# Kernel optimization log

Measured on AMD Instinct MI355X. Metric: run time of the kernel, lower is better.

Reference implementation:

```python
import jax, jax.numpy as jnp
import numpy as np

B, S, HID, NH, K = 4, 1500, 1024, 16, 64
DH = HID // NH  # 64


def _rel_bias(pos_emb, length):
    # pos_emb: [2K+1, d]; Shaw-style relative position embedding lookup -> [S, S, d]
    kk = (pos_emb.shape[0] - 1) // 2
    idx = jnp.arange(length)
    dist = jnp.clip(idx[None, :] - idx[:, None], -kk, kk) + kk
    return pos_emb[dist]


def setup_inputs() -> dict:
    key = jax.random.key(0)
    ks = jax.random.split(key, 12)
    sq = 1.0 / np.sqrt(HID)
    inp = {
        "query": jax.random.normal(ks[0], (B, S, HID), jnp.float32),
        "key": jax.random.normal(ks[1], (B, S, HID), jnp.float32),
        "value": jax.random.normal(ks[2], (B, S, HID), jnp.float32),
        # per-head QKV projections stacked over heads: [NH, HID, DH]
        "Wq": jax.random.normal(ks[3], (NH, HID, DH), jnp.float32) * sq,
        "bq": jnp.zeros((NH, DH), jnp.float32),
        "Wk": jax.random.normal(ks[4], (NH, HID, DH), jnp.float32) * sq,
        "bk": jnp.zeros((NH, DH), jnp.float32),
        "Wv": jax.random.normal(ks[5], (NH, HID, DH), jnp.float32) * sq,
        "bv": jnp.zeros((NH, DH), jnp.float32),
        # relative position tables [2K+1, DH]
        "pos_k": jax.random.normal(ks[6], (2 * K + 1, DH), jnp.float32) * 0.1,
        "pos_v": jax.random.normal(ks[7], (2 * K + 1, DH), jnp.float32) * 0.1,
        # output projection
        "W_fc": jax.random.normal(ks[8], (HID, HID), jnp.float32) * sq,
        "b_fc": jnp.zeros((HID,), jnp.float32),
    }
    return inp


def reference(query, key, value, Wq, bq, Wk, bk, Wv, bv, pos_k, pos_v, W_fc, b_fc):
    seq = query.shape[1]
    k_bias = _rel_bias(pos_k, seq)  # [S, S, DH]
    v_bias = _rel_bias(pos_v, seq)  # [S, S, DH]

    # batched per-head projections: [B, NH, S, DH]
    q = jnp.einsum('bsh,nhd->bnsd', query, Wq) + bq[None, :, None, :]
    k = jnp.einsum('bsh,nhd->bnsd', key, Wk) + bk[None, :, None, :]
    v = jnp.einsum('bsh,nhd->bnsd', value, Wv) + bv[None, :, None, :]

    attn_1 = jnp.einsum('bnqd,bnkd->bnqk', q, k)
    attn_2 = jnp.einsum('bnqd,qkd->bnqk', q, k_bias)  # Shaw relative key bias
    scores = (attn_1 + attn_2) / jnp.sqrt(jnp.float32(DH))
    w = jax.nn.softmax(scores, axis=-1)  # [B, NH, S, S]

    values_1 = jnp.einsum('bnqk,bnkd->bnqd', w, v)
    values_2 = jnp.einsum('bnqk,qkd->bnqd', w, v_bias)  # Shaw relative value bias
    heads = values_1 + values_2  # [B, NH, S, DH]

    # concat heads in head order -> [B, S, HID]
    hidden = jnp.transpose(heads, (0, 2, 1, 3)).reshape(query.shape[0], seq, -1)
    return hidden @ W_fc + b_fc
```

## Files before the change

### kernel.cpp

```cpp
#include <hip/hip_runtime.h>
#include <stdint.h>

typedef unsigned short u16;
typedef __attribute__((ext_vector_type(8))) short bf16x8;
typedef __attribute__((ext_vector_type(4))) float f32x4;

#define MFMA16(a, b, c) __builtin_amdgcn_mfma_f32_16x16x32_bf16(a, b, c, 0, 0, 0)

__device__ __forceinline__ u16 f2bf(float x) {
  union { float f; uint32_t u; } v; v.f = x;
  uint32_t r = (v.u + 0x7FFFu + ((v.u >> 16) & 1u)) >> 16;
  return (u16)r;
}
__device__ __forceinline__ float bf2f(u16 h) {
  union { uint32_t u; float f; } v; v.u = ((uint32_t)h) << 16; return v.f;
}
__device__ __forceinline__ void gll16(const void* g, void* s) {
  __builtin_amdgcn_global_load_lds((const __attribute__((address_space(1))) unsigned int*)g,
                                   (__attribute__((address_space(3))) unsigned int*)s, 16, 0, 0);
}


__global__ __launch_bounds__(256) void pack_x_kernel(const float* __restrict__ q,
                                                     const float* __restrict__ k,
                                                     const float* __restrict__ v,
                                                     u16* __restrict__ X) {
  const float* src = blockIdx.z == 0 ? q : (blockIdx.z == 1 ? k : v);
  u16* dst = X + (size_t)blockIdx.z * (6016UL * 1024UL);
  size_t idx = (size_t)blockIdx.x * 1024 + (size_t)threadIdx.x * 4;
  float4 f = *(const float4*)(src + idx);
  ushort4 o;
  o.x = f2bf(f.x); o.y = f2bf(f.y); o.z = f2bf(f.z); o.w = f2bf(f.w);
  *(ushort4*)(dst + idx) = o;
}

__global__ __launch_bounds__(256) void pack_misc_kernel(const float* __restrict__ bq,
                                                        const float* __restrict__ bk,
                                                        const float* __restrict__ bv,
                                                        const float* __restrict__ posk,
                                                        const float* __restrict__ posv,
                                                        float* __restrict__ biascat,
                                                        u16* __restrict__ poskbf,
                                                        u16* __restrict__ posvT) {
  for (int i = threadIdx.x; i < 1024; i += 256) {
    biascat[i] = bq[i]; biascat[1024 + i] = bk[i]; biascat[2048 + i] = bv[i];
  }
  for (int i = threadIdx.x; i < 144 * 64; i += 256) {
    int r = i >> 6;
    poskbf[i] = (r < 129) ? f2bf(posk[i]) : (u16)0;
  }
  {
    const int d = threadIdx.x & 63, rr = threadIdx.x >> 6;
#pragma unroll
    for (int j = 0; j < 34; ++j) {
      const int r = rr * 34 + j;
      posvT[d * 136 + r] = (r < 129) ? f2bf(posv[(size_t)r * 64 + d]) : (u16)0;
    }
  }
}

__global__ __launch_bounds__(256) void pack_wqkv_kernel(const float* __restrict__ Wq,
                                                        const float* __restrict__ Wk,
                                                        const float* __restrict__ Wv,
                                                        u16* __restrict__ Wt) {
  __shared__ float tile[64][65];
  const float* W = blockIdx.z == 0 ? Wq : (blockIdx.z == 1 ? Wk : Wv);
  u16* dst = Wt + (size_t)blockIdx.z * (1024UL * 1024UL);
  const int n = blockIdx.y, h0 = blockIdx.x * 64;
  const int r = threadIdx.x >> 2, c0 = (threadIdx.x & 3) * 16;
  const float* src = W + (size_t)n * 65536 + (size_t)(h0 + r) * 64 + c0;
#pragma unroll
  for (int j = 0; j < 16; j += 4) {
    float4 f = *(const float4*)(src + j);
    tile[r][c0 + j] = f.x; tile[r][c0 + j + 1] = f.y;
    tile[r][c0 + j + 2] = f.z; tile[r][c0 + j + 3] = f.w;
  }
  __syncthreads();
  u16* outp = dst + (size_t)(n * 64 + r) * 1024 + h0 + c0;
#pragma unroll
  for (int j = 0; j < 16; ++j) outp[j] = f2bf(tile[c0 + j][r]);
}

__global__ __launch_bounds__(256) void pack_wfc_kernel(const float* __restrict__ Wfc,
                                                       u16* __restrict__ Wfct) {
  __shared__ float tile[64][65];
  const int i0 = blockIdx.x * 64, o0 = blockIdx.y * 64;
  const int r = threadIdx.x >> 2, c0 = (threadIdx.x & 3) * 16;
  const float* src = Wfc + (size_t)(i0 + r) * 1024 + o0 + c0;
#pragma unroll
  for (int j = 0; j < 16; j += 4) {
    float4 f = *(const float4*)(src + j);
    tile[r][c0 + j] = f.x; tile[r][c0 + j + 1] = f.y;
    tile[r][c0 + j + 2] = f.z; tile[r][c0 + j + 3] = f.w;
  }
  __syncthreads();
  u16* outp = Wfct + (size_t)(o0 + r) * 1024 + i0 + c0;
#pragma unroll
  for (int j = 0; j < 16; ++j) outp[j] = f2bf(tile[c0 + j][r]);
}

__global__ __launch_bounds__(256) void vtrans_kernel(const u16* __restrict__ qkv,
                                                     u16* __restrict__ Vt) {
  const size_t ZS = 4UL * 16 * 1536 * 64;
  __shared__ u16 t[64][72];
  const int bh = blockIdx.x & 63, s0 = (blockIdx.x >> 6) * 64;
  const u16* src = qkv + 2 * ZS + (size_t)bh * (1536UL * 64UL) + (size_t)s0 * 64;
  const int r = threadIdx.x >> 2, c0 = (threadIdx.x & 3) * 16;
  *(uint4*)&t[r][c0]     = *(const uint4*)(src + (size_t)r * 64 + c0);
  *(uint4*)&t[r][c0 + 8] = *(const uint4*)(src + (size_t)r * 64 + c0 + 8);
  __syncthreads();
  uint4 a, bvec;
  uint tmp[8];
#pragma unroll
  for (int j = 0; j < 8; ++j)
    tmp[j] = (uint)t[c0 + 2 * j][r] | ((uint)t[c0 + 2 * j + 1][r] << 16);
  a.x = tmp[0]; a.y = tmp[1]; a.z = tmp[2]; a.w = tmp[3];
  bvec.x = tmp[4]; bvec.y = tmp[5]; bvec.z = tmp[6]; bvec.w = tmp[7];
  u16* dst = Vt + (size_t)(bh * 64 + r) * 1536 + s0 + c0;
  *(uint4*)dst = a;
  *(uint4*)(dst + 8) = bvec;
}

__global__ __launch_bounds__(256) void gemm_bt_kernel(
    const u16* __restrict__ Abase, long aStride,
    const u16* __restrict__ Bbase, long bStride,
    const float* __restrict__ biasBase, long biasStride,
    u16* __restrict__ outBF, float* __restrict__ outF, int mode) {
  const int z = blockIdx.z;
  const u16* A = Abase + (size_t)z * aStride;
  const u16* Bt = Bbase + (size_t)z * bStride;
  const float* bias = biasBase + (size_t)z * biasStride;
  __shared__ u16 As[128 * 32];
  __shared__ u16 Bs[128 * 32];
  const int tid = threadIdx.x, w = tid >> 6, lane = tid & 63;
  const int quad = lane >> 4, l16 = lane & 15;
  const int wm = w >> 1, wn = w & 1;
  const int m0 = blockIdx.y * 128, n0 = blockIdx.x * 128;
  const int srow = w * 16 + (lane >> 2);
  const int scol = (lane & 3) * 8;
  const u16* gA0 = A + (size_t)(m0 + srow) * 1024 + scol;
  const u16* gA1 = gA0 + 64UL * 1024;
  const u16* gB0 = Bt + (size_t)(n0 + srow) * 1024 + scol;
  const u16* gB1 = gB0 + 64UL * 1024;
  u16* lA0 = As + (w * 16) * 32;
  u16* lA1 = As + (64 + w * 16) * 32;
  u16* lB0 = Bs + (w * 16) * 32;
  u16* lB1 = Bs + (64 + w * 16) * 32;

  f32x4 acc[4][4];
  const f32x4 zf = {0.f, 0.f, 0.f, 0.f};
#pragma unroll
  for (int a = 0; a < 4; ++a)
#pragma unroll
    for (int b = 0; b < 4; ++b) acc[a][b] = zf;

  for (int kt = 0; kt < 32; ++kt) {
    const int k0 = kt * 32;
    gll16(gA0 + k0, lA0);
    gll16(gA1 + k0, lA1);
    gll16(gB0 + k0, lB0);
    gll16(gB1 + k0, lB1);
    __syncthreads();
    bf16x8 af[4], bfr[4];
#pragma unroll
    for (int f = 0; f < 4; ++f) {
      af[f]  = *(const bf16x8*)(As + (wm * 64 + f * 16 + l16) * 32 + quad * 8);
      bfr[f] = *(const bf16x8*)(Bs + (wn * 64 + f * 16 + l16) * 32 + quad * 8);
    }
#pragma unroll
    for (int fm = 0; fm < 4; ++fm)
#pragma unroll
      for (int fn = 0; fn < 4; ++fn)
        acc[fm][fn] = MFMA16(af[fm], bfr[fn], acc[fm][fn]);
    __syncthreads();
  }

  if (mode == 0) {
    const float scale = (z == 0) ? 0.125f : 1.0f;
    u16* out = outBF + (size_t)z * (4UL * 16 * 1536 * 64);
#pragma unroll
    for (int fm = 0; fm < 4; ++fm) {
#pragma unroll
      for (int i = 0; i < 4; ++i) {
        const int m = m0 + wm * 64 + fm * 16 + quad * 4 + i;
        if (m >= 6000) continue;
        const int bb = m / 1500;
        const int s = m - bb * 1500;
#pragma unroll
        for (int fn = 0; fn < 4; ++fn) {
          const int n = n0 + wn * 64 + fn * 16 + l16;
          const float vv = (acc[fm][fn][i] + bias[n]) * scale;
          const int h = n >> 6, d = n & 63;
          out[((size_t)(bb * 16 + h) * 1536 + s) * 64 + d] = f2bf(vv);
        }
      }
    }
  } else {
#pragma unroll
    for (int fm = 0; fm < 4; ++fm) {
#pragma unroll
      for (int i = 0; i < 4; ++i) {
        const int m = m0 + wm * 64 + fm * 16 + quad * 4 + i;
        if (m >= 6000) continue;
#pragma unroll
        for (int fn = 0; fn < 4; ++fn) {
          const int n = n0 + wn * 64 + fn * 16 + l16;
          outF[(size_t)m * 1024 + n] = acc[fm][fn][i] + bias[n];
        }
      }
    }
  }
}

__global__ __launch_bounds__(256) void attn_kernel(const u16* __restrict__ qkv,
                                                   const u16* __restrict__ Vt,
                                                   const u16* __restrict__ poskbf,
                                                   const u16* __restrict__ posvT,
                                                   const float* __restrict__ posv,
                                                   u16* __restrict__ hidden) {
  const size_t ZS = 4UL * 16 * 1536 * 64;
  __shared__ u16 qp_s[64 * 136];
  __shared__ u16 pb_s[64 * 136];
  __shared__ u16 kbuf[2][2048];
  __shared__ u16 vbuf[2][2048];

  const int tid = threadIdx.x;
  const int w = tid >> 6, lane = tid & 63, quad = lane >> 4, l16 = lane & 15;
  const int bi = blockIdx.x;
  const int bh = bi & 63;
  const int q0 = (bi >> 6) * 64, qw0 = q0 + w * 16;
  const int b = bh >> 4;
  const size_t sb = (size_t)bh * (1536UL * 64UL);
  const u16* Qp = qkv + sb;
  const u16* Kp = qkv + ZS + sb;
  const u16* Vtb = Vt + (size_t)bh * (64UL * 1536UL);
  u16* qp_row = qp_s + (w * 16 + l16) * 136;
  u16* pb_row = pb_s + (w * 16 + l16) * 136;

  const int r8 = lane >> 3, c8 = lane & 7;
  const int vr = lane >> 2, vc = lane & 3;
  auto stageK = [&](int it, int buf) {
    const u16* src = Kp + (size_t)(it * 32 + w * 8 + r8) * 64 + ((c8 ^ r8) * 8);
    gll16(src, &kbuf[buf][w * 512]);
  };
  auto stageV = [&](int it, int buf) {
    const u16* src = Vtb + (size_t)(w * 16 + vr) * 1536 + it * 32 + vc * 8;
    gll16(src, &vbuf[buf][w * 512]);
  };

  {
    uint* pz = (uint*)(pb_s + w * 16 * 136);
    for (int i = lane; i < 1088; i += 64) pz[i] = 0u;
  }

  stageK(0, 0);
  stageV(0, 0);

  const u16* qptr = Qp + (size_t)(qw0 + l16) * 64 + quad * 8;
  const bf16x8 qB0 = *(const bf16x8*)qptr;
  const bf16x8 qB1 = *(const bf16x8*)(qptr + 32);

  const f32x4 zf = {0.f, 0.f, 0.f, 0.f};
#pragma unroll
  for (int nf = 0; nf < 9; ++nf) {
    const u16* bp = poskbf + (size_t)(nf * 16 + l16) * 64 + quad * 8;
    bf16x8 b0 = *(const bf16x8*)bp;
    bf16x8 b1 = *(const bf16x8*)(bp + 32);
    f32x4 c = zf;
    c = MFMA16(qB0, b0, c);
    c = MFMA16(qB1, b1, c);
    const int col = nf * 16 + l16;
    if (col < 136) {
#pragma unroll
      for (int i = 0; i < 4; ++i)
        qp_s[(w * 16 + quad * 4 + i) * 136 + col] = f2bf(c[i]);
    }
  }
  __syncthreads();

  const float L2E = 1.44269504f;
  const float M8 = -8.0f * L2E;
  const float eLow  = __builtin_fmaf(bf2f(qp_row[0]), L2E, M8);
  const float eHigh = __builtin_fmaf(bf2f(qp_row[128]), L2E, M8);

  f32x4 accf[4];
#pragma unroll
  for (int dc = 0; dc < 4; ++dc) accf[dc] = zf;
  float sSimple = 0.f, sLowSave = 0.f, sDall = 0.f, sD0 = 0.f, sD128 = 0.f;

  const int itLowEnd = (qw0 >= 95) ? (((qw0 - 95) >> 5) + 1) : 0;
  const int itHigh0 = (qw0 + 110) >> 5;
  const int dEnd = itHigh0 < 46 ? itHigh0 : 46;

  const int kswz = (quad ^ (l16 & 7)) * 8;
  const int kswz4 = ((quad + 4) ^ (l16 & 7)) * 8;
  const int laneLo = ((quad & 1) << 5) + l16;
  const bool cgHi = quad >= 2;

  for (int it = 0; it < 47; ++it) {
    const int cur = it & 1;
    if (it < 46) { stageK(it + 1, cur ^ 1); stageV(it + 1, cur ^ 1); }

    if (it == itLowEnd) sLowSave = sSimple;
    const int phase = (it < itLowEnd) ? 0 : ((it >= 46) ? 1 : ((it < dEnd) ? 1 : 2));

    const u16* kb = kbuf[cur];
    bf16x8 ka00 = *(const bf16x8*)(kb + l16 * 64 + kswz);
    bf16x8 ka01 = *(const bf16x8*)(kb + l16 * 64 + kswz4);
    bf16x8 ka10 = *(const bf16x8*)(kb + (16 + l16) * 64 + kswz);
    bf16x8 ka11 = *(const bf16x8*)(kb + (16 + l16) * 64 + kswz4);
    const u16* vbse = vbuf[cur];
    bf16x8 vb0 = *(const bf16x8*)(vbse + l16 * 32 + quad * 8);
    bf16x8 vb1 = *(const bf16x8*)(vbse + (16 + l16) * 32 + quad * 8);
    bf16x8 vb2 = *(const bf16x8*)(vbse + (32 + l16) * 32 + quad * 8);
    bf16x8 vb3 = *(const bf16x8*)(vbse + (48 + l16) * 32 + quad * 8);

    float qb[2][4];
    if (phase == 1) {
      const int base = it * 32 + 64 - qw0 - l16;
#pragma unroll
      for (int cg = 0; cg < 2; ++cg) {
#pragma unroll
        for (int i = 0; i < 4; ++i) {
          int delta = base + cg * 16 + quad * 4 + i;
          delta = delta < 0 ? 0 : (delta > 128 ? 128 : delta);
          qb[cg][i] = bf2f(qp_row[delta]);
        }
      }
    }

    f32x4 cc[2];
    cc[0] = zf; cc[1] = zf;
    cc[0] = MFMA16(ka00, qB0, cc[0]);
    cc[0] = MFMA16(ka01, qB1, cc[0]);
    cc[1] = MFMA16(ka10, qB0, cc[1]);
    cc[1] = MFMA16(ka11, qB1, cc[1]);

    float pvv[2][4];
    if (phase != 1) {
      const float eB = (phase == 0) ? eLow : eHigh;
#pragma unroll
      for (int cg = 0; cg < 2; ++cg) {
#pragma unroll
        for (int i = 0; i < 4; ++i) {
          float p = __builtin_amdgcn_exp2f(__builtin_fmaf(cc[cg][i], L2E, eB));
          sSimple += p; pvv[cg][i] = p;
        }
      }
    } else {
      const int kc0 = it * 32;
#pragma unroll
      for (int cg = 0; cg < 2; ++cg) {
        const int krow0 = kc0 + cg * 16 + quad * 4;
        const int dbase = krow0 + 64 - qw0 - l16;
#pragma unroll
        for (int i = 0; i < 4; ++i) {
          int delta = dbase + i;
          delta = delta < 0 ? 0 : (delta > 128 ? 128 : delta);
          const float t = cc[cg][i] + qb[cg][i];
          float p = __builtin_amdgcn_exp2f(__builtin_fmaf(t, L2E, M8));
          if (krow0 + i >= 1500) p = 0.f;
          sDall += p;
          sD0   += (delta == 0)   ? p : 0.f;
          sD128 += (delta == 128) ? p : 0.f;
          if ((delta != 0) & (delta != 128)) pb_row[delta] = f2bf(p);
          pvv[cg][i] = p;
        }
      }
    }

    const uint u00 = (uint)f2bf(pvv[0][0]) | ((uint)f2bf(pvv[0][1]) << 16);
    const uint u01 = (uint)f2bf(pvv[0][2]) | ((uint)f2bf(pvv[0][3]) << 16);
    const uint u10 = (uint)f2bf(pvv[1][0]) | ((uint)f2bf(pvv[1][1]) << 16);
    const uint u11 = (uint)f2bf(pvv[1][2]) | ((uint)f2bf(pvv[1][3]) << 16);
    const uint lo00 = __shfl(u00, laneLo),      lo01 = __shfl(u01, laneLo);
    const uint lo10 = __shfl(u10, laneLo),      lo11 = __shfl(u11, laneLo);
    const uint hi00 = __shfl(u00, laneLo + 16), hi01 = __shfl(u01, laneLo + 16);
    const uint hi10 = __shfl(u10, laneLo + 16), hi11 = __shfl(u11, laneLo + 16);
    union { uint u[4]; bf16x8 v; } pa;
    pa.u[0] = cgHi ? lo10 : lo00;
    pa.u[1] = cgHi ? lo11 : lo01;
    pa.u[2] = cgHi ? hi10 : hi00;
    pa.u[3] = cgHi ? hi11 : hi01;

    accf[0] = MFMA16(pa.v, vb0, accf[0]);
    accf[1] = MFMA16(pa.v, vb1, accf[1]);
    accf[2] = MFMA16(pa.v, vb2, accf[2]);
    accf[3] = MFMA16(pa.v, vb3, accf[3]);

    __syncthreads();
  }

  const float sLow = sLowSave;
  const float sHigh = sSimple - sLowSave;
  float lpart = sSimple + sDall;
  float clow = sLow + sD0;
  float chigh = sHigh + sD128;
#pragma unroll
  for (int m = 16; m <= 32; m <<= 1) {
    lpart += __shfl_xor(lpart, m);
    clow  += __shfl_xor(clow, m);
    chigh += __shfl_xor(chigh, m);
  }
  const float linv = 1.0f / lpart;

  f32x4 o2[4];
#pragma unroll
  for (int dc = 0; dc < 4; ++dc) o2[dc] = zf;
  const u16* pbr = pb_s + (w * 16 + l16) * 136;
#pragma unroll
  for (int kk = 0; kk < 4; ++kk) {
    bf16x8 pa2 = *(const bf16x8*)(pbr + kk * 32 + quad * 8);
#pragma unroll
    for (int dc = 0; dc < 4; ++dc) {
      bf16x8 vb2r = *(const bf16x8*)(posvT + (size_t)(dc * 16 + l16) * 136 + kk * 32 + quad * 8);
      o2[dc] = MFMA16(pa2, vb2r, o2[dc]);
    }
  }

  float li[4], cl[4], ch[4];
#pragma unroll
  for (int i = 0; i < 4; ++i) {
    const int srcl = quad * 4 + i;
    li[i] = __shfl(linv, srcl);
    cl[i] = __shfl(clow, srcl);
    ch[i] = __shfl(chigh, srcl);
  }

#pragma unroll
  for (int dc = 0; dc < 4; ++dc) {
    const int d = dc * 16 + l16;
    const float pv0 = posv[d], pv1 = posv[128 * 64 + d];
#pragma unroll
    for (int i = 0; i < 4; ++i) {
      const int qg = qw0 + quad * 4 + i;
      if (qg < 1500) {
        const float val = (accf[dc][i] + o2[dc][i] + cl[i] * pv0 + ch[i] * pv1) * li[i];
        hidden[((size_t)(b * 1500 + qg)) * 1024 + (bh & 15) * 64 + d] = f2bf(val);
      }
    }
  }
}

extern "C" void kernel_launch(void* const* d_in, const int* in_sizes, int n_in,
                              void* d_out, int out_size, void* d_ws, size_t ws_size,
                              hipStream_t stream) {
  const float* query = (const float*)d_in[0];
  const float* key   = (const float*)d_in[1];
  const float* value = (const float*)d_in[2];
  const float* Wq = (const float*)d_in[3];
  const float* bq = (const float*)d_in[4];
  const float* Wk = (const float*)d_in[5];
  const float* bk = (const float*)d_in[6];
  const float* Wv = (const float*)d_in[7];
  const float* bv = (const float*)d_in[8];
  const float* posk = (const float*)d_in[9];
  const float* posv = (const float*)d_in[10];
  const float* Wfc = (const float*)d_in[11];
  const float* bfc = (const float*)d_in[12];
  float* out = (float*)d_out;

  char* p = (char*)d_ws;
  u16* X = (u16*)p;        p += 3UL * 6016 * 1024 * 2;
  u16* Wt = (u16*)p;       p += 3UL * 1024 * 1024 * 2;
  u16* Wfct = (u16*)p;     p += 1024UL * 1024 * 2;
  u16* poskbf = (u16*)p;   p += 144UL * 64 * 2;
  u16* posvT = (u16*)p;    p += 64UL * 136 * 2;
  float* biascat = (float*)p; p += 3UL * 1024 * 4;
  u16* qkv = (u16*)p;      p += 3UL * 4 * 16 * 1536 * 64 * 2;
  u16* hidden = X;
  u16* Vt = X + 6291456;

  pack_x_kernel<<<dim3(6000, 1, 3), 256, 0, stream>>>(query, key, value, X);
  pack_misc_kernel<<<dim3(1), 256, 0, stream>>>(bq, bk, bv, posk, posv, biascat, poskbf, posvT);
  pack_wqkv_kernel<<<dim3(16, 16, 3), 256, 0, stream>>>(Wq, Wk, Wv, Wt);
  pack_wfc_kernel<<<dim3(16, 16), 256, 0, stream>>>(Wfc, Wfct);

  gemm_bt_kernel<<<dim3(8, 47, 3), 256, 0, stream>>>(
      X, 6016L * 1024, Wt, 1024L * 1024, biascat, 1024L, qkv, nullptr, 0);

  vtrans_kernel<<<dim3(1536), 256, 0, stream>>>(qkv, Vt);

  attn_kernel<<<dim3(1536), 256, 0, stream>>>(qkv, Vt, poskbf, posvT, posv, hidden);

  gemm_bt_kernel<<<dim3(8, 47, 1), 256, 0, stream>>>(
      hidden, 0L, Wfct, 0L, bfc, 0L, nullptr, out, 1);
}
```

Before: 394.2 us.

## Merge weight pack kernels, swizzle V tile in LDS, use packed bf16 conversion

Folds the three small weight and misc packing kernels into one launch that dispatches on block index, cutting launch count. It XOR-swizzles the V tile column offset on both the global-to-LDS staging and the MFMA read to reduce LDS bank conflicts. It also replaces the manual bf16 rounding with the hardware v_cvt_pk_bf16_f32 instruction in the input pack and in the attention softmax, where the relative-bias probability scatter now reuses the packed values. The inline asm ties the code to targets that have this instruction, and its rounding has to match the software round-to-nearest-even.

```diff
diff --git a/kernel.cpp b/kernel.cpp
--- a/kernel.cpp
+++ b/kernel.cpp
@@ -14,6 +14,11 @@
 }
 __device__ __forceinline__ float bf2f(u16 h) {
   union { uint32_t u; float f; } v; v.u = ((uint32_t)h) << 16; return v.f;
+}
+__device__ __forceinline__ uint cvt_pk_bf16(float a, float b) {
+  uint r;
+  asm("v_cvt_pk_bf16_f32 %0, %1, %2" : "=v"(r) : "v"(a), "v"(b));
+  return r;
 }
 __device__ __forceinline__ void gll16(const void* g, void* s) {
   __builtin_amdgcn_global_load_lds((const __attribute__((address_space(1))) unsigned int*)g,
@@ -29,46 +34,58 @@
   u16* dst = X + (size_t)blockIdx.z * (6016UL * 1024UL);
   size_t idx = (size_t)blockIdx.x * 1024 + (size_t)threadIdx.x * 4;
   float4 f = *(const float4*)(src + idx);
-  ushort4 o;
-  o.x = f2bf(f.x); o.y = f2bf(f.y); o.z = f2bf(f.z); o.w = f2bf(f.w);
-  *(ushort4*)(dst + idx) = o;
-}
-
-__global__ __launch_bounds__(256) void pack_misc_kernel(const float* __restrict__ bq,
-                                                        const float* __restrict__ bk,
-                                                        const float* __restrict__ bv,
-                                                        const float* __restrict__ posk,
-                                                        const float* __restrict__ posv,
-                                                        float* __restrict__ biascat,
-                                                        u16* __restrict__ poskbf,
-                                                        u16* __restrict__ posvT) {
-  for (int i = threadIdx.x; i < 1024; i += 256) {
-    biascat[i] = bq[i]; biascat[1024 + i] = bk[i]; biascat[2048 + i] = bv[i];
-  }
-  for (int i = threadIdx.x; i < 144 * 64; i += 256) {
-    int r = i >> 6;
-    poskbf[i] = (r < 129) ? f2bf(posk[i]) : (u16)0;
-  }
-  {
+  uint2 o;
+  o.x = cvt_pk_bf16(f.x, f.y);
+  o.y = cvt_pk_bf16(f.z, f.w);
+  *(uint2*)(dst + idx) = o;
+}
+
+__global__ __launch_bounds__(256) void pack_w_kernel(const float* __restrict__ Wq,
+                                                     const float* __restrict__ Wk,
+                                                     const float* __restrict__ Wv,
+                                                     const float* __restrict__ Wfc,
+                                                     const float* __restrict__ bq,
+                                                     const float* __restrict__ bk,
+                                                     const float* __restrict__ bv,
+                                                     const float* __restrict__ posk,
+                                                     const float* __restrict__ posv,
+                                                     u16* __restrict__ Wt,
+                                                     u16* __restrict__ Wfct,
+                                                     float* __restrict__ biascat,
+                                                     u16* __restrict__ poskbf,
+                                                     u16* __restrict__ posvT) {
+  __shared__ float tile[64][65];
+  const int bi = blockIdx.x;
+  if (bi == 1024) {
+    for (int i = threadIdx.x; i < 1024; i += 256) {
+      biascat[i] = bq[i]; biascat[1024 + i] = bk[i]; biascat[2048 + i] = bv[i];
+    }
+    for (int i = threadIdx.x; i < 144 * 64; i += 256) {
+      int r = i >> 6;
+      poskbf[i] = (r < 129) ? f2bf(posk[i]) : (u16)0;
+    }
     const int d = threadIdx.x & 63, rr = threadIdx.x >> 6;
 #pragma unroll
     for (int j = 0; j < 34; ++j) {
       const int r = rr * 34 + j;
       posvT[d * 136 + r] = (r < 129) ? f2bf(posv[(size_t)r * 64 + d]) : (u16)0;
     }
-  }
-}
-
-__global__ __launch_bounds__(256) void pack_wqkv_kernel(const float* __restrict__ Wq,
-                                                        const float* __restrict__ Wk,
-                                                        const float* __restrict__ Wv,
-                                                        u16* __restrict__ Wt) {
-  __shared__ float tile[64][65];
-  const float* W = blockIdx.z == 0 ? Wq : (blockIdx.z == 1 ? Wk : Wv);
-  u16* dst = Wt + (size_t)blockIdx.z * (1024UL * 1024UL);
-  const int n = blockIdx.y, h0 = blockIdx.x * 64;
+    return;
+  }
   const int r = threadIdx.x >> 2, c0 = (threadIdx.x & 3) * 16;
-  const float* src = W + (size_t)n * 65536 + (size_t)(h0 + r) * 64 + c0;
+  const float* src;
+  u16* outp;
+  if (bi < 768) {
+    const int z = bi >> 8, rem = bi & 255, n = rem >> 4, h0 = (rem & 15) * 64;
+    const float* W = z == 0 ? Wq : (z == 1 ? Wk : Wv);
+    src = W + (size_t)n * 65536 + (size_t)(h0 + r) * 64 + c0;
+    outp = Wt + (size_t)z * (1024UL * 1024UL) + (size_t)(n * 64 + r) * 1024 + h0 + c0;
+  } else {
+    const int t = bi - 768;
+    const int i0 = (t & 15) * 64, o0 = (t >> 4) * 64;
+    src = Wfc + (size_t)(i0 + r) * 1024 + o0 + c0;
+    outp = Wfct + (size_t)(o0 + r) * 1024 + i0 + c0;
+  }
 #pragma unroll
   for (int j = 0; j < 16; j += 4) {
     float4 f = *(const float4*)(src + j);
@@ -76,25 +93,6 @@
     tile[r][c0 + j + 2] = f.z; tile[r][c0 + j + 3] = f.w;
   }
   __syncthreads();
-  u16* outp = dst + (size_t)(n * 64 + r) * 1024 + h0 + c0;
-#pragma unroll
-  for (int j = 0; j < 16; ++j) outp[j] = f2bf(tile[c0 + j][r]);
-}
-
-__global__ __launch_bounds__(256) void pack_wfc_kernel(const float* __restrict__ Wfc,
-                                                       u16* __restrict__ Wfct) {
-  __shared__ float tile[64][65];
-  const int i0 = blockIdx.x * 64, o0 = blockIdx.y * 64;
-  const int r = threadIdx.x >> 2, c0 = (threadIdx.x & 3) * 16;
-  const float* src = Wfc + (size_t)(i0 + r) * 1024 + o0 + c0;
-#pragma unroll
-  for (int j = 0; j < 16; j += 4) {
-    float4 f = *(const float4*)(src + j);
-    tile[r][c0 + j] = f.x; tile[r][c0 + j + 1] = f.y;
-    tile[r][c0 + j + 2] = f.z; tile[r][c0 + j + 3] = f.w;
-  }
-  __syncthreads();
-  u16* outp = Wfct + (size_t)(o0 + r) * 1024 + i0 + c0;
 #pragma unroll
   for (int j = 0; j < 16; ++j) outp[j] = f2bf(tile[c0 + j][r]);
 }
@@ -244,7 +242,7 @@
     gll16(src, &kbuf[buf][w * 512]);
   };
   auto stageV = [&](int it, int buf) {
-    const u16* src = Vtb + (size_t)(w * 16 + vr) * 1536 + it * 32 + vc * 8;
+    const u16* src = Vtb + (size_t)(w * 16 + vr) * 1536 + it * 32 + ((vc ^ ((vr >> 1) & 3)) * 8);
     gll16(src, &vbuf[buf][w * 512]);
   };
 
@@ -294,6 +292,7 @@
 
   const int kswz = (quad ^ (l16 & 7)) * 8;
   const int kswz4 = ((quad + 4) ^ (l16 & 7)) * 8;
+  const int vpos = (quad ^ ((l16 >> 1) & 3)) * 8;
   const int laneLo = ((quad & 1) << 5) + l16;
   const bool cgHi = quad >= 2;
 
@@ -310,10 +309,10 @@
     bf16x8 ka10 = *(const bf16x8*)(kb + (16 + l16) * 64 + kswz);
     bf16x8 ka11 = *(const bf16x8*)(kb + (16 + l16) * 64 + kswz4);
     const u16* vbse = vbuf[cur];
-    bf16x8 vb0 = *(const bf16x8*)(vbse + l16 * 32 + quad * 8);
-    bf16x8 vb1 = *(const bf16x8*)(vbse + (16 + l16) * 32 + quad * 8);
-    bf16x8 vb2 = *(const bf16x8*)(vbse + (32 + l16) * 32 + quad * 8);
-    bf16x8 vb3 = *(const bf16x8*)(vbse + (48 + l16) * 32 + quad * 8);
+    bf16x8 vb0 = *(const bf16x8*)(vbse + l16 * 32 + vpos);
+    bf16x8 vb1 = *(const bf16x8*)(vbse + (16 + l16) * 32 + vpos);
+    bf16x8 vb2 = *(const bf16x8*)(vbse + (32 + l16) * 32 + vpos);
+    bf16x8 vb3 = *(const bf16x8*)(vbse + (48 + l16) * 32 + vpos);
 
     float qb[2][4];
     if (phase == 1) {
@@ -363,16 +362,24 @@
           sDall += p;
           sD0   += (delta == 0)   ? p : 0.f;
           sD128 += (delta == 128) ? p : 0.f;
-          if ((delta != 0) & (delta != 128)) pb_row[delta] = f2bf(p);
           pvv[cg][i] = p;
         }
-      }
-    }
-
-    const uint u00 = (uint)f2bf(pvv[0][0]) | ((uint)f2bf(pvv[0][1]) << 16);
-    const uint u01 = (uint)f2bf(pvv[0][2]) | ((uint)f2bf(pvv[0][3]) << 16);
-    const uint u10 = (uint)f2bf(pvv[1][0]) | ((uint)f2bf(pvv[1][1]) << 16);
-    const uint u11 = (uint)f2bf(pvv[1][2]) | ((uint)f2bf(pvv[1][3]) << 16);
+        const uint pk01 = cvt_pk_bf16(pvv[cg][0], pvv[cg][1]);
+        const uint pk23 = cvt_pk_bf16(pvv[cg][2], pvv[cg][3]);
+        const u16 hb[4] = {(u16)pk01, (u16)(pk01 >> 16), (u16)pk23, (u16)(pk23 >> 16)};
+#pragma unroll
+        for (int i = 0; i < 4; ++i) {
+          int delta = dbase + i;
+          delta = delta < 0 ? 0 : (delta > 128 ? 128 : delta);
+          if ((delta != 0) & (delta != 128)) pb_row[delta] = hb[i];
+        }
+      }
+    }
+
+    const uint u00 = cvt_pk_bf16(pvv[0][0], pvv[0][1]);
+    const uint u01 = cvt_pk_bf16(pvv[0][2], pvv[0][3]);
+    const uint u10 = cvt_pk_bf16(pvv[1][0], pvv[1][1]);
+    const uint u11 = cvt_pk_bf16(pvv[1][2], pvv[1][3]);
     const uint lo00 = __shfl(u00, laneLo),      lo01 = __shfl(u01, laneLo);
     const uint lo10 = __shfl(u10, laneLo),      lo11 = __shfl(u11, laneLo);
     const uint hi00 = __shfl(u00, laneLo + 16), hi01 = __shfl(u01, laneLo + 16);
@@ -472,9 +479,8 @@
   u16* Vt = X + 6291456;
 
   pack_x_kernel<<<dim3(6000, 1, 3), 256, 0, stream>>>(query, key, value, X);
-  pack_misc_kernel<<<dim3(1), 256, 0, stream>>>(bq, bk, bv, posk, posv, biascat, poskbf, posvT);
-  pack_wqkv_kernel<<<dim3(16, 16, 3), 256, 0, stream>>>(Wq, Wk, Wv, Wt);
-  pack_wfc_kernel<<<dim3(16, 16), 256, 0, stream>>>(Wfc, Wfct);
+  pack_w_kernel<<<dim3(1025), 256, 0, stream>>>(Wq, Wk, Wv, Wfc, bq, bk, bv, posk, posv,
+                                                Wt, Wfct, biascat, poskbf, posvT);
 
   gemm_bt_kernel<<<dim3(8, 47, 3), 256, 0, stream>>>(
       X, 6016L * 1024, Wt, 1024L * 1024, biascat, 1024L, qkv, nullptr, 0);
```

Measured after the change: 382.8 us. 2.9% less time.
